# Performance work log

Hardware: AMD Instinct MI355X
Metric: run time of the kernel (lower is better)

## Reference

```python
import jax, jax.numpy as jnp
import numpy as np
from jax import lax

B, C, H, W = 8, 256, 128, 128


def _scan_along(x, decay, axis):
    """Linear decay recurrence s_t = decay*s_{t-1} + (1-decay)*x_t along `axis`.

    x: [B, C, H, W]; decay: [C] (constant per channel).
    """
    xm = jnp.moveaxis(x, axis, 0)          # [L, B, C, rest]
    d = decay.reshape(1, -1, 1)            # broadcast over [B, C, rest]
    one_minus_d = 1.0 - d

    def step(state, cur):
        state = d * state + one_minus_d * cur
        return state, state

    init = jnp.zeros_like(xm[0])
    _, ys = lax.scan(step, init, xm)
    return jnp.moveaxis(ys, 0, axis)


def setup_inputs() -> dict:
    key = jax.random.key(0)
    k1, k2, k3, k4 = jax.random.split(key, 4)
    x = jax.random.normal(k1, (B, C, H, W), dtype=jnp.float32)
    decay_logits = 0.5 * jax.random.normal(k2, (4, C), dtype=jnp.float32)
    mix_logits = 0.5 * jax.random.normal(k3, (4, C), dtype=jnp.float32)
    input_scale = 0.5 * jax.random.normal(k4, (4, C), dtype=jnp.float32)
    return {"x": x, "decay_logits": decay_logits,
            "mix_logits": mix_logits, "input_scale": input_scale}


def reference(x, decay_logits, mix_logits, input_scale):
    decay = jnp.clip(jax.nn.sigmoid(decay_logits), 0.05, 0.995)   # [4, C]
    mix = jax.nn.softmax(mix_logits, axis=0)                       # [4, C]
    scale = 1.0 + jnp.tanh(input_scale)                            # [4, C]

    def sc(d):  # per-channel [C] -> broadcastable [1, C, 1, 1]
        return d.reshape(1, -1, 1, 1)

    # left -> right: scan along width (axis 3)
    lr = _scan_along(x * sc(scale[0]), decay[0], axis=3)
    # right -> left: flip width, scan, flip back
    rl = jnp.flip(_scan_along(jnp.flip(x, axis=3) * sc(scale[1]), decay[1], axis=3), axis=3)
    # top -> bottom: scan along height (axis 2)
    tb = _scan_along(x * sc(scale[2]), decay[2], axis=2)
    # bottom -> top: flip height, scan, flip back
    bt = jnp.flip(_scan_along(jnp.flip(x, axis=2) * sc(scale[3]), decay[3], axis=2), axis=2)

    return sc(mix[0]) * lr + sc(mix[1]) * rl + sc(mix[2]) * tb + sc(mix[3]) * bt
```

## Files before the change

### kernel.cpp

```cpp
#include <hip/hip_runtime.h>

#define CH 256
#define HH 128
#define WW 128
#define HW (HH * WW)
#define SEGH 16
#define NSEG 8

__global__ __launch_bounds__(1024, 4) void dscan_kernel(
    const float* __restrict__ x,
    const float* __restrict__ decay_logits,
    const float* __restrict__ mix_logits,
    const float* __restrict__ input_scale,
    float* __restrict__ out)
{
    __shared__ float xs[HW];

    const int img  = blockIdx.x;
    const int c    = img & (CH - 1);
    const int tid  = threadIdx.x;
    const int lane = tid & 63;
    const int wv   = tid >> 6;

    const float dl0 = decay_logits[0 * CH + c];
    const float dl1 = decay_logits[1 * CH + c];
    const float dl2 = decay_logits[2 * CH + c];
    const float dl3 = decay_logits[3 * CH + c];
    const float ml0 = mix_logits[0 * CH + c];
    const float ml1 = mix_logits[1 * CH + c];
    const float ml2 = mix_logits[2 * CH + c];
    const float ml3 = mix_logits[3 * CH + c];
    const float il0 = input_scale[0 * CH + c];
    const float il1 = input_scale[1 * CH + c];
    const float il2 = input_scale[2 * CH + c];
    const float il3 = input_scale[3 * CH + c];

    const float d0 = fminf(fmaxf(1.0f / (1.0f + expf(-dl0)), 0.05f), 0.995f);
    const float d1 = fminf(fmaxf(1.0f / (1.0f + expf(-dl1)), 0.05f), 0.995f);
    const float d2 = fminf(fmaxf(1.0f / (1.0f + expf(-dl2)), 0.05f), 0.995f);
    const float d3 = fminf(fmaxf(1.0f / (1.0f + expf(-dl3)), 0.05f), 0.995f);

    const float mmax = fmaxf(fmaxf(ml0, ml1), fmaxf(ml2, ml3));
    const float e0 = expf(ml0 - mmax);
    const float e1 = expf(ml1 - mmax);
    const float e2 = expf(ml2 - mmax);
    const float e3 = expf(ml3 - mmax);
    const float einv = 1.0f / (e0 + e1 + e2 + e3);
    const float m0 = e0 * einv, m1 = e1 * einv, m2 = e2 * einv, m3 = e3 * einv;

    const float sc0 = 1.0f + tanhf(il0);
    const float sc1 = 1.0f + tanhf(il1);
    const float sc2 = 1.0f + tanhf(il2);
    const float sc3 = 1.0f + tanhf(il3);

    const float c0 = (1.0f - d0) * sc0;
    const float c1 = (1.0f - d1) * sc1;
    const float c2 = (1.0f - d2) * sc2;
    const float c3 = (1.0f - d3) * sc3;

    const float d0p4 = (d0 * d0) * (d0 * d0);
    const float d1p4 = (d1 * d1) * (d1 * d1);
    float t2 = d2 * d2; t2 = t2 * t2; t2 = t2 * t2; const float d2p16 = t2 * t2;
    float t3 = d3 * d3; t3 = t3 * t3; t3 = t3 * t3; const float d3p16 = t3 * t3;

    const float* __restrict__ xg = x + (size_t)img * HW;
    float* __restrict__ og = out + (size_t)img * HW;

    const int col = tid & (WW - 1);
    const int seg = tid >> 7;
    const float* __restrict__ xcol = xg + seg * SEGH * WW + col;

    {
        float b2 = 0.0f, b3 = 0.0f, pw = c3;
#pragma unroll
        for (int i = 0; i < SEGH; ++i) {
            const float xv = xcol[i * WW];
            b2 = fmaf(d2, b2, c2 * xv);
            b3 = fmaf(pw, xv, b3);
            pw *= d3;
        }
        xs[tid]        = b2;
        xs[1024 + tid] = b3;
    }
    __syncthreads();

    float Sin = 0.0f;
    for (int j = 0; j < seg; ++j)
        Sin = fmaf(d2p16, Sin, xs[j * WW + col]);
    float Tin = 0.0f;
    for (int j = NSEG - 1; j > seg; --j)
        Tin = fmaf(d3p16, Tin, xs[1024 + j * WW + col]);
    __syncthreads();

    {
        const int sl   = lane & 31;
        const int half = lane >> 5;
#pragma unroll
        for (int it = 0; it < 4; ++it) {
            const int r = (((it << 4) + wv) << 1) + half;
            const float4 xv4 = *(const float4*)(xg + r * WW + (sl << 2));

            float bL = c0 * xv4.x;
            bL = fmaf(d0, bL, c0 * xv4.y);
            bL = fmaf(d0, bL, c0 * xv4.z);
            bL = fmaf(d0, bL, c0 * xv4.w);
            float aL = d0p4;
            float bR = c1 * xv4.w;
            bR = fmaf(d1, bR, c1 * xv4.z);
            bR = fmaf(d1, bR, c1 * xv4.y);
            bR = fmaf(d1, bR, c1 * xv4.x);
            float aR = d1p4;

#pragma unroll
            for (int off = 1; off < 32; off <<= 1) {
                const float aU = __shfl_up(aL, (unsigned)off, 32);
                const float bU = __shfl_up(bL, (unsigned)off, 32);
                if (sl >= off) { bL = fmaf(aL, bU, bL); aL *= aU; }
                const float aD = __shfl_down(aR, (unsigned)off, 32);
                const float bD = __shfl_down(bR, (unsigned)off, 32);
                if (sl < 32 - off) { bR = fmaf(aR, bD, bR); aR *= aD; }
            }
            float EL = __shfl_up(bL, 1u, 32);
            if (sl == 0) EL = 0.0f;
            float ER = __shfl_down(bR, 1u, 32);
            if (sl == 31) ER = 0.0f;

            const float l0 = fmaf(d0, EL, c0 * xv4.x);
            const float l1 = fmaf(d0, l0, c0 * xv4.y);
            const float l2 = fmaf(d0, l1, c0 * xv4.z);
            const float l3 = fmaf(d0, l2, c0 * xv4.w);
            const float r3 = fmaf(d1, ER, c1 * xv4.w);
            const float r2 = fmaf(d1, r3, c1 * xv4.z);
            const float r1 = fmaf(d1, r2, c1 * xv4.y);
            const float r0 = fmaf(d1, r1, c1 * xv4.x);

            float4 o4;
            o4.x = fmaf(m0, l0, m1 * r0);
            o4.y = fmaf(m0, l1, m1 * r1);
            o4.z = fmaf(m0, l2, m1 * r2);
            o4.w = fmaf(m0, l3, m1 * r3);
            *(float4*)(xs + r * WW + (sl << 2)) = o4;
        }
    }
    __syncthreads();

    {
        float xv[SEGH], tb[SEGH];
        float s = Sin;
#pragma unroll
        for (int i = 0; i < SEGH; ++i) {
            const float v = xcol[i * WW];
            xv[i] = v;
            s = fmaf(d2, s, c2 * v);
            tb[i] = s;
        }
        float t = Tin;
        float* __restrict__ ocol = og + seg * SEGH * WW + col;
        const float* __restrict__ pcol = xs + seg * SEGH * WW + col;
#pragma unroll
        for (int i = SEGH - 1; i >= 0; --i) {
            t = fmaf(d3, t, c3 * xv[i]);
            const float hres = pcol[i * WW];
            ocol[i * WW] = fmaf(m2, tb[i], fmaf(m3, t, hres));
        }
    }
}

extern "C" void kernel_launch(void* const* d_in, const int* in_sizes, int n_in,
                              void* d_out, int out_size, void* d_ws, size_t ws_size,
                              hipStream_t stream) {
    const float* x  = (const float*)d_in[0];
    const float* dl = (const float*)d_in[1];
    const float* ml = (const float*)d_in[2];
    const float* is = (const float*)d_in[3];
    float* out = (float*)d_out;

    dim3 grid(2048), block(1024);
    hipLaunchKernelGGL(dscan_kernel, grid, block, 0, stream, x, dl, ml, is, out);
}
```

Baseline: 260.7 us.

## Merge vertical carry pass with horizontal scan, precompute shuffle decay powers

```diff
diff --git a/kernel.cpp b/kernel.cpp
--- a/kernel.cpp
+++ b/kernel.cpp
@@ -14,7 +14,9 @@
     const float* __restrict__ input_scale,
     float* __restrict__ out)
 {
-    __shared__ float xs[HW];
+    extern __shared__ float smem[];
+    float* __restrict__ xs  = smem;
+    float* __restrict__ scr = smem + HW;
 
     const int img  = blockIdx.x;
     const int c    = img & (CH - 1);
@@ -60,65 +62,48 @@
 
     const float d0p4 = (d0 * d0) * (d0 * d0);
     const float d1p4 = (d1 * d1) * (d1 * d1);
+    float q0[5], q1[5];
+    q0[0] = d0p4; q1[0] = d1p4;
+#pragma unroll
+    for (int k = 1; k < 5; ++k) { q0[k] = q0[k-1] * q0[k-1]; q1[k] = q1[k-1] * q1[k-1]; }
+
     float t2 = d2 * d2; t2 = t2 * t2; t2 = t2 * t2; const float d2p16 = t2 * t2;
     float t3 = d3 * d3; t3 = t3 * t3; t3 = t3 * t3; const float d3p16 = t3 * t3;
 
     const float* __restrict__ xg = x + (size_t)img * HW;
     float* __restrict__ og = out + (size_t)img * HW;
 
-    const int col = tid & (WW - 1);
-    const int seg = tid >> 7;
-    const float* __restrict__ xcol = xg + seg * SEGH * WW + col;
-
-    {
-        float b2 = 0.0f, b3 = 0.0f, pw = c3;
-#pragma unroll
-        for (int i = 0; i < SEGH; ++i) {
-            const float xv = xcol[i * WW];
-            b2 = fmaf(d2, b2, c2 * xv);
-            b3 = fmaf(pw, xv, b3);
-            pw *= d3;
-        }
-        xs[tid]        = b2;
-        xs[1024 + tid] = b3;
-    }
-    __syncthreads();
-
-    float Sin = 0.0f;
-    for (int j = 0; j < seg; ++j)
-        Sin = fmaf(d2p16, Sin, xs[j * WW + col]);
-    float Tin = 0.0f;
-    for (int j = NSEG - 1; j > seg; --j)
-        Tin = fmaf(d3p16, Tin, xs[1024 + j * WW + col]);
-    __syncthreads();
-
     {
         const int sl   = lane & 31;
         const int half = lane >> 5;
+        const int rbase = (wv << 1) + half;
+
+        float4 v[4];
+#pragma unroll
+        for (int it = 0; it < 4; ++it)
+            v[it] = *(const float4*)(xg + ((it << 5) + rbase) * WW + (sl << 2));
+
 #pragma unroll
         for (int it = 0; it < 4; ++it) {
-            const int r = (((it << 4) + wv) << 1) + half;
-            const float4 xv4 = *(const float4*)(xg + r * WW + (sl << 2));
+            const int r = (it << 5) + rbase;
+            const float4 xv4 = v[it];
 
             float bL = c0 * xv4.x;
             bL = fmaf(d0, bL, c0 * xv4.y);
             bL = fmaf(d0, bL, c0 * xv4.z);
             bL = fmaf(d0, bL, c0 * xv4.w);
-            float aL = d0p4;
             float bR = c1 * xv4.w;
             bR = fmaf(d1, bR, c1 * xv4.z);
             bR = fmaf(d1, bR, c1 * xv4.y);
             bR = fmaf(d1, bR, c1 * xv4.x);
-            float aR = d1p4;
 
 #pragma unroll
-            for (int off = 1; off < 32; off <<= 1) {
-                const float aU = __shfl_up(aL, (unsigned)off, 32);
+            for (int k = 0; k < 5; ++k) {
+                const int off = 1 << k;
                 const float bU = __shfl_up(bL, (unsigned)off, 32);
-                if (sl >= off) { bL = fmaf(aL, bU, bL); aL *= aU; }
-                const float aD = __shfl_down(aR, (unsigned)off, 32);
+                bL = fmaf(q0[k], (sl >= off) ? bU : 0.0f, bL);
                 const float bD = __shfl_down(bR, (unsigned)off, 32);
-                if (sl < 32 - off) { bR = fmaf(aR, bD, bR); aR *= aD; }
+                bR = fmaf(q1[k], (sl < 32 - off) ? bD : 0.0f, bR);
             }
             float EL = __shfl_up(bL, 1u, 32);
             if (sl == 0) EL = 0.0f;
@@ -142,7 +127,31 @@
             *(float4*)(xs + r * WW + (sl << 2)) = o4;
         }
     }
+
+    const int col = tid & (WW - 1);
+    const int seg = tid >> 7;
+    const float* __restrict__ xcol = xg + seg * SEGH * WW + col;
+    {
+        float b2 = 0.0f, b3 = 0.0f, pw = c3;
+#pragma unroll
+        for (int i = 0; i < SEGH; ++i) {
+            const float xv = xcol[i * WW];
+            b2 = fmaf(d2, b2, c2 * xv);
+            b3 = fmaf(pw, xv, b3);
+            pw *= d3;
+        }
+        scr[tid]        = b2;
+        scr[1024 + tid] = b3;
+    }
+
     __syncthreads();
+
+    float Sin = 0.0f;
+    for (int j = 0; j < seg; ++j)
+        Sin = fmaf(d2p16, Sin, scr[j * WW + col]);
+    float Tin = 0.0f;
+    for (int j = NSEG - 1; j > seg; --j)
+        Tin = fmaf(d3p16, Tin, scr[1024 + j * WW + col]);
 
     {
         float xv[SEGH], tb[SEGH];
@@ -175,6 +184,16 @@
     const float* is = (const float*)d_in[3];
     float* out = (float*)d_out;
 
+    const size_t lds_bytes = (size_t)(HW + 2048) * sizeof(float);
+
+    static bool attr_set = false;
+    if (!attr_set) {
+        (void)hipFuncSetAttribute((const void*)dscan_kernel,
+                                  hipFuncAttributeMaxDynamicSharedMemorySize,
+                                  (int)lds_bytes);
+        attr_set = true;
+    }
+
     dim3 grid(2048), block(1024);
-    hipLaunchKernelGGL(dscan_kernel, grid, block, 0, stream, x, dl, ml, is, out);
+    hipLaunchKernelGGL(dscan_kernel, grid, block, lds_bytes, stream, x, dl, ml, is, out);
 }
```

New measurement: 245.4 us. 1.06x faster.
